# Performance work log

Measured on AMD Instinct MI355X. Metric: run time of the kernel, lower is better.

The kernel has to match this reference:

```python
import jax, jax.numpy as jnp
import numpy as np

N_NODES = 10000
N_EDGES = 320000
D_FEAT = 512
N_HIDDEN = 256
N_LATENT = 64


def setup_inputs() -> dict:
    key = jax.random.key(0)
    ks = jax.random.split(key, 7)
    x = jax.random.normal(ks[0], (N_NODES, D_FEAT), dtype=jnp.float32)
    edge_src = jax.random.randint(ks[1], (N_EDGES,), 0, N_NODES, dtype=jnp.int32)
    edge_dst = jax.random.randint(ks[2], (N_EDGES,), 0, N_NODES, dtype=jnp.int32)
    # positive weights, like D^{-1/2} A D^{-1/2} entries
    edge_weight = jax.random.uniform(ks[3], (N_EDGES,), dtype=jnp.float32)
    scale1 = 1.0 / np.sqrt(D_FEAT)
    scale2 = 1.0 / np.sqrt(N_HIDDEN)
    W1 = jax.random.normal(ks[4], (D_FEAT, N_HIDDEN), dtype=jnp.float32) * scale1
    W2_mu = jax.random.normal(ks[5], (N_HIDDEN, N_LATENT), dtype=jnp.float32) * scale2
    W2_sig = jax.random.normal(ks[6], (N_HIDDEN, N_LATENT), dtype=jnp.float32) * scale2
    return {"x": x, "edge_src": edge_src, "edge_dst": edge_dst,
            "edge_weight": edge_weight, "W1": W1, "W2_mu": W2_mu, "W2_sig": W2_sig}


def reference(x, edge_src, edge_dst, edge_weight, W1, W2_mu, W2_sig):
    N = x.shape[0]

    def spmm(feat):
        # sparse adj_norm @ feat via gather + weighted segment-sum
        msg = feat[edge_src] * edge_weight[:, None]           # [E, F]
        return jax.ops.segment_sum(msg, edge_dst, num_segments=N)  # [N, F]

    # GCN layer 1: relu(adj @ (x @ W1)); dropout is identity at inference
    h = jax.nn.relu(spmm(x @ W1))                              # [N, H]
    # GCN layer 2 (mu and log-sigma heads); encoder returns exp(log_sig)
    mu = spmm(h @ W2_mu)                                       # [N, L]
    sigma = jnp.exp(spmm(h @ W2_sig))                          # [N, L]
    # InnerProductDecoder: adj = z @ z.T (normalized z_ is computed but unused
    # in the original code, so it is faithfully omitted); z = mu embedding
    adj_rec = mu @ mu.T                                        # [N, N]
    return mu, sigma, adj_rec
```

## Files before the change

kernel.cpp:

```cpp
#include <hip/hip_runtime.h>
#include <hip/hip_bf16.h>
#include <math.h>
#include <float.h>

#define N_NODES 10000
#define N_EDGES 320000
#define D_FEAT  512
#define N_HID   256
#define N_LAT   64


__global__ __launch_bounds__(256) void k_hist(const int* __restrict__ dst,
                                              int* __restrict__ deg) {
    int i = blockIdx.x * 256 + threadIdx.x;
    if (i < N_EDGES) atomicAdd(&deg[dst[i]], 1);
}

__global__ __launch_bounds__(1024) void k_scan(const int* __restrict__ deg,
                                               int* __restrict__ rowptr,
                                               int* __restrict__ woff) {
    __shared__ int wsum[16];
    __shared__ int carry_s;
    int tid = threadIdx.x;
    if (tid == 0) carry_s = 0;
    __syncthreads();
    int lane = tid & 63, wv = tid >> 6;
    for (int base = 0; base < N_NODES; base += 1024) {
        int i = base + tid;
        int v = (i < N_NODES) ? deg[i] : 0;
        int x = v;
        #pragma unroll
        for (int off = 1; off < 64; off <<= 1) {
            int y = __shfl_up(x, off);
            if (lane >= off) x += y;
        }
        if (lane == 63) wsum[wv] = x;
        __syncthreads();
        int add = carry_s;
        for (int k = 0; k < wv; k++) add += wsum[k];
        int incl = x + add;
        int excl = incl - v;
        if (i < N_NODES) { rowptr[i] = excl; woff[i] = excl; }
        __syncthreads();
        if (tid == 1023) carry_s = incl;
        __syncthreads();
    }
    if (tid == 0) rowptr[N_NODES] = carry_s;
}

__global__ __launch_bounds__(256) void k_scatter(const int* __restrict__ src,
                                                 const int* __restrict__ dst,
                                                 const float* __restrict__ w,
                                                 int* __restrict__ woff,
                                                 int* __restrict__ esrc,
                                                 float* __restrict__ ew) {
    int i = blockIdx.x * 256 + threadIdx.x;
    if (i < N_EDGES) {
        int d = dst[i];
        int r = atomicAdd(&woff[d], 1);
        esrc[r] = src[i];
        ew[r] = w[i];
    }
}


__global__ __launch_bounds__(256) void k_gemm1(const float* __restrict__ x,
                                               const float* __restrict__ W1,
                                               float* __restrict__ xw1) {
    __shared__ float xs[16][33];
    int j = threadIdx.x;
    int r0 = blockIdx.x * 16;
    float acc[16];
    #pragma unroll
    for (int r = 0; r < 16; r++) acc[r] = 0.f;

    for (int kc = 0; kc < D_FEAT; kc += 32) {
        #pragma unroll
        for (int t = 0; t < 2; t++) {
            int idx = j + t * 256;
            int rr = idx >> 5, kk = idx & 31;
            int row = r0 + rr;
            xs[rr][kk] = (row < N_NODES) ? x[row * D_FEAT + kc + kk] : 0.f;
        }
        __syncthreads();
        #pragma unroll
        for (int kk = 0; kk < 32; kk++) {
            float b = W1[(kc + kk) * N_HID + j];
            #pragma unroll
            for (int r = 0; r < 16; r++) acc[r] += xs[r][kk] * b;
        }
        __syncthreads();
    }
    #pragma unroll
    for (int r = 0; r < 16; r++) {
        int row = r0 + r;
        if (row < N_NODES) xw1[row * N_HID + j] = acc[r];
    }
}


__global__ __launch_bounds__(256) void k_spmm1(const int* __restrict__ rowptr,
                                               const int* __restrict__ esrc,
                                               const float* __restrict__ ew,
                                               const float* __restrict__ xw1,
                                               float* __restrict__ h) {
    int n = blockIdx.x;
    int tid = threadIdx.x;
    int s = rowptr[n], e = rowptr[n + 1];
    float acc = 0.f;
    for (int i = s; i < e; i++) {
        int sc = esrc[i];
        float wv = ew[i];
        acc += wv * xw1[sc * N_HID + tid];
    }
    h[n * N_HID + tid] = fmaxf(acc, 0.f);
}


__global__ __launch_bounds__(256) void k_gemm2(const float* __restrict__ h,
                                               const float* __restrict__ W2mu,
                                               const float* __restrict__ W2sig,
                                               float* __restrict__ pre) {
    __shared__ float hs[32][33];
    int tid = threadIdx.x;
    int j = tid & 127;
    int half = tid >> 7;
    int r0 = blockIdx.x * 32;
    const float* B = (j < 64) ? W2mu : W2sig;
    int jj = j & 63;
    float acc[16];
    #pragma unroll
    for (int r = 0; r < 16; r++) acc[r] = 0.f;

    for (int kc = 0; kc < N_HID; kc += 32) {
        #pragma unroll
        for (int t = 0; t < 4; t++) {
            int idx = tid + t * 256;
            int rr = idx >> 5, kk = idx & 31;
            int row = r0 + rr;
            hs[rr][kk] = (row < N_NODES) ? h[row * N_HID + kc + kk] : 0.f;
        }
        __syncthreads();
        int rb = half * 16;
        #pragma unroll
        for (int kk = 0; kk < 32; kk++) {
            float b = B[(kc + kk) * N_LAT + jj];
            #pragma unroll
            for (int r = 0; r < 16; r++) acc[r] += hs[rb + r][kk] * b;
        }
        __syncthreads();
    }
    #pragma unroll
    for (int r = 0; r < 16; r++) {
        int row = r0 + half * 16 + r;
        if (row < N_NODES) pre[row * 128 + j] = acc[r];
    }
}


__global__ __launch_bounds__(128) void k_spmm2(const int* __restrict__ rowptr,
                                               const int* __restrict__ esrc,
                                               const float* __restrict__ ew,
                                               const float* __restrict__ pre,
                                               float* __restrict__ out_mu,
                                               float* __restrict__ out_sig) {
    int n = blockIdx.x;
    int tid = threadIdx.x;
    int lane = tid & 63, wv = tid >> 6;
    int s = rowptr[n], e = rowptr[n + 1];
    const float* p = pre + wv * 64 + lane;
    float acc = 0.f;
    for (int i = s; i < e; i++) {
        acc += ew[i] * p[esrc[i] * 128];
    }
    if (wv == 0) {
        out_mu[n * 64 + lane] = acc;
    } else {
        float sgv = fminf(expf(acc), 3.0e38f);
        out_sig[n * 64 + lane] = sgv;
    }
}


typedef __bf16 bf16x4 __attribute__((ext_vector_type(4)));
typedef __bf16 bf16x8 __attribute__((ext_vector_type(8)));
typedef float  f32x4  __attribute__((ext_vector_type(4)));

__global__ __launch_bounds__(256) void k_mu2bf(const float* __restrict__ mu,
                                               __bf16* __restrict__ muh,
                                               __bf16* __restrict__ mul) {
    int i = blockIdx.x * 256 + threadIdx.x;
    float4 v = ((const float4*)mu)[i];
    __bf16 h0 = (__bf16)v.x, h1 = (__bf16)v.y, h2 = (__bf16)v.z, h3 = (__bf16)v.w;
    __bf16 l0 = (__bf16)(v.x - (float)h0);
    __bf16 l1 = (__bf16)(v.y - (float)h1);
    __bf16 l2 = (__bf16)(v.z - (float)h2);
    __bf16 l3 = (__bf16)(v.w - (float)h3);
    bf16x4 hv = {h0, h1, h2, h3};
    bf16x4 lv = {l0, l1, l2, l3};
    ((bf16x4*)muh)[i] = hv;
    ((bf16x4*)mul)[i] = lv;
}


#define ADJ_TS 68

__global__ __launch_bounds__(256) void k_adj(const __bf16* __restrict__ muh,
                                             const __bf16* __restrict__ mul,
                                             float* __restrict__ C) {
    __shared__ float Ts[4][32 * ADJ_TS];
    int tid = threadIdx.x;
    int l = tid & 63, w = tid >> 6;
    int wr = w >> 1, wc = w & 1;
    int i0 = blockIdx.y * 128 + wr * 64;
    int j0 = blockIdx.x * 128 + wc * 64;
    int lr = l & 15;
    int lk = (l >> 4) * 8;

    f32x4 acc[4][4];
    #pragma unroll
    for (int a = 0; a < 4; a++)
        #pragma unroll
        for (int b = 0; b < 4; b++) acc[a][b] = (f32x4)(0.0f);

    #pragma unroll
    for (int ks = 0; ks < 2; ks++) {
        int k0 = ks * 32 + lk;
        bf16x8 ah[4], al[4], bh[4], bl[4];
        #pragma unroll
        for (int mi = 0; mi < 4; mi++) {
            int row = i0 + mi * 16 + lr;
            if (row > N_NODES - 1) row = N_NODES - 1;
            ah[mi] = *(const bf16x8*)(muh + row * 64 + k0);
            al[mi] = *(const bf16x8*)(mul + row * 64 + k0);
        }
        #pragma unroll
        for (int ni = 0; ni < 4; ni++) {
            int row = j0 + ni * 16 + lr;
            if (row > N_NODES - 1) row = N_NODES - 1;
            bh[ni] = *(const bf16x8*)(muh + row * 64 + k0);
            bl[ni] = *(const bf16x8*)(mul + row * 64 + k0);
        }
        #pragma unroll
        for (int mi = 0; mi < 4; mi++)
            #pragma unroll
            for (int ni = 0; ni < 4; ni++) {
                acc[mi][ni] = __builtin_amdgcn_mfma_f32_16x16x32_bf16(ah[mi], bh[ni], acc[mi][ni], 0, 0, 0);
                acc[mi][ni] = __builtin_amdgcn_mfma_f32_16x16x32_bf16(ah[mi], bl[ni], acc[mi][ni], 0, 0, 0);
                acc[mi][ni] = __builtin_amdgcn_mfma_f32_16x16x32_bf16(al[mi], bh[ni], acc[mi][ni], 0, 0, 0);
            }
    }

    float* T = Ts[w];
    int c16 = l & 15, r4 = l >> 4;
    #pragma unroll
    for (int half = 0; half < 2; half++) {
        __syncthreads();
        #pragma unroll
        for (int m2 = 0; m2 < 2; m2++) {
            int mi = half * 2 + m2;
            #pragma unroll
            for (int ni = 0; ni < 4; ni++)
                #pragma unroll
                for (int r = 0; r < 4; r++)
                    T[(m2 * 16 + r4 * 4 + r) * ADJ_TS + ni * 16 + c16] = acc[mi][ni][r];
        }
        __syncthreads();
        #pragma unroll
        for (int q = 0; q < 8; q++) {
            int rr = q * 4 + r4;
            int row = i0 + half * 32 + rr;
            int col = j0 + c16 * 4;
            if (row < N_NODES && col < N_NODES)
                *(float4*)&C[(size_t)row * N_NODES + col] =
                    *(const float4*)&T[rr * ADJ_TS + c16 * 4];
        }
    }
}


extern "C" void kernel_launch(void* const* d_in, const int* in_sizes, int n_in,
                              void* d_out, int out_size, void* d_ws, size_t ws_size,
                              hipStream_t stream) {
    const float* x       = (const float*)d_in[0];
    const int*   esrc_in = (const int*)d_in[1];
    const int*   edst_in = (const int*)d_in[2];
    const float* ew_in   = (const float*)d_in[3];
    const float* W1      = (const float*)d_in[4];
    const float* W2mu    = (const float*)d_in[5];
    const float* W2sig   = (const float*)d_in[6];

    char* ws = (char*)d_ws;
    float* xw1    = (float*)(ws + 0);
    float* h      = (float*)(ws + 10240000);
    float* pre    = (float*)(ws + 20480000);
    int*   esrc   = (int*)  (ws + 25600000);
    float* ew     = (float*)(ws + 26880000);
    int*   deg    = (int*)  (ws + 28160000);
    int*   rowptr = (int*)  (ws + 28200000);
    int*   woff   = (int*)  (ws + 28240016);

    __bf16* muh = (__bf16*)(ws + 0);
    __bf16* mul = (__bf16*)(ws + 1280000);

    float* out_mu  = (float*)d_out;
    float* out_sig = out_mu + 640000;
    float* out_adj = out_sig + 640000;

    hipMemsetAsync(deg, 0, N_NODES * sizeof(int), stream);
    k_hist   <<<(N_EDGES + 255) / 256, 256, 0, stream>>>(edst_in, deg);
    k_scan   <<<1, 1024, 0, stream>>>(deg, rowptr, woff);
    k_scatter<<<(N_EDGES + 255) / 256, 256, 0, stream>>>(esrc_in, edst_in, ew_in,
                                                         woff, esrc, ew);
    k_gemm1  <<<N_NODES / 16, 256, 0, stream>>>(x, W1, xw1);
    k_spmm1  <<<N_NODES, 256, 0, stream>>>(rowptr, esrc, ew, xw1, h);
    k_gemm2  <<<(N_NODES + 31) / 32, 256, 0, stream>>>(h, W2mu, W2sig, pre);
    k_spmm2  <<<N_NODES, 128, 0, stream>>>(rowptr, esrc, ew, pre, out_mu, out_sig);
    k_mu2bf  <<<640000 / 4 / 256, 256, 0, stream>>>(out_mu, muh, mul);
    dim3 gadj((N_NODES + 127) / 128, (N_NODES + 127) / 128);
    k_adj    <<<gadj, 256, 0, stream>>>(muh, mul, out_adj);
}
```

Before: 787.6 us.

## Use split-bf16 MFMA for dense GEMMs and wave-per-node vectorized SpMM

The two dense GEMMs (x@W1 and h@W2) move from scalar FP32 FMA loops to bf16 MFMA with a hi/lo split (three products) to keep near-FP32 accuracy. New kernels pre-split x and the weights into bf16 hi/lo parts, and SpMM1 now emits h directly as bf16 hi/lo. The SpMMs are rewritten to one wavefront per node with float4/float2 vector gathers and a 4-way unrolled edge loop, replacing one block per node. This adds split and conversion passes and extra workspace traffic in exchange for matrix-core throughput and fewer, wider memory transactions.

```diff
diff --git a/kernel.cpp b/kernel.cpp
--- a/kernel.cpp
+++ b/kernel.cpp
@@ -8,6 +8,10 @@
 #define D_FEAT  512
 #define N_HID   256
 #define N_LAT   64
+
+typedef __bf16 bf16x4 __attribute__((ext_vector_type(4)));
+typedef __bf16 bf16x8 __attribute__((ext_vector_type(8)));
+typedef float  f32x4  __attribute__((ext_vector_type(4)));
 
 
 __global__ __launch_bounds__(256) void k_hist(const int* __restrict__ dst,
@@ -64,127 +68,238 @@
 }
 
 
-__global__ __launch_bounds__(256) void k_gemm1(const float* __restrict__ x,
-                                               const float* __restrict__ W1,
-                                               float* __restrict__ xw1) {
-    __shared__ float xs[16][33];
-    int j = threadIdx.x;
-    int r0 = blockIdx.x * 16;
-    float acc[16];
-    #pragma unroll
-    for (int r = 0; r < 16; r++) acc[r] = 0.f;
-
-    for (int kc = 0; kc < D_FEAT; kc += 32) {
-        #pragma unroll
-        for (int t = 0; t < 2; t++) {
-            int idx = j + t * 256;
-            int rr = idx >> 5, kk = idx & 31;
-            int row = r0 + rr;
-            xs[rr][kk] = (row < N_NODES) ? x[row * D_FEAT + kc + kk] : 0.f;
-        }
-        __syncthreads();
-        #pragma unroll
-        for (int kk = 0; kk < 32; kk++) {
-            float b = W1[(kc + kk) * N_HID + j];
-            #pragma unroll
-            for (int r = 0; r < 16; r++) acc[r] += xs[r][kk] * b;
-        }
-        __syncthreads();
-    }
-    #pragma unroll
-    for (int r = 0; r < 16; r++) {
-        int row = r0 + r;
-        if (row < N_NODES) xw1[row * N_HID + j] = acc[r];
-    }
-}
-
-
-__global__ __launch_bounds__(256) void k_spmm1(const int* __restrict__ rowptr,
-                                               const int* __restrict__ esrc,
-                                               const float* __restrict__ ew,
-                                               const float* __restrict__ xw1,
-                                               float* __restrict__ h) {
-    int n = blockIdx.x;
+__global__ __launch_bounds__(256) void k_xsplit(const float* __restrict__ x,
+                                                __bf16* __restrict__ xh,
+                                                __bf16* __restrict__ xl) {
+    int i = blockIdx.x * 256 + threadIdx.x;
+    float4 v = ((const float4*)x)[i];
+    __bf16 h0 = (__bf16)v.x, h1 = (__bf16)v.y, h2 = (__bf16)v.z, h3 = (__bf16)v.w;
+    bf16x4 hv = {h0, h1, h2, h3};
+    bf16x4 lv = {(__bf16)(v.x - (float)h0), (__bf16)(v.y - (float)h1),
+                 (__bf16)(v.z - (float)h2), (__bf16)(v.w - (float)h3)};
+    ((bf16x4*)xh)[i] = hv;
+    ((bf16x4*)xl)[i] = lv;
+}
+
+__global__ __launch_bounds__(256) void k_wsplit(const float* __restrict__ W1,
+                                                const float* __restrict__ W2mu,
+                                                const float* __restrict__ W2sig,
+                                                __bf16* __restrict__ w1h,
+                                                __bf16* __restrict__ w1l,
+                                                __bf16* __restrict__ w2h,
+                                                __bf16* __restrict__ w2l) {
+    int i = blockIdx.x * 256 + threadIdx.x;
+    if (i < 512 * 256) {
+        int j = i >> 9, k = i & 511;
+        float v = W1[k * N_HID + j];
+        __bf16 hi = (__bf16)v;
+        w1h[i] = hi;
+        w1l[i] = (__bf16)(v - (float)hi);
+    } else {
+        int t = i - 512 * 256;
+        int j = t >> 8, k = t & 255;
+        float v = (j < 64) ? W2mu[k * N_LAT + j] : W2sig[k * N_LAT + (j - 64)];
+        __bf16 hi = (__bf16)v;
+        w2h[t] = hi;
+        w2l[t] = (__bf16)(v - (float)hi);
+    }
+}
+
+
+__global__ __launch_bounds__(256) void k_gemm1m(const __bf16* __restrict__ xh,
+                                                const __bf16* __restrict__ xl,
+                                                const __bf16* __restrict__ w1h,
+                                                const __bf16* __restrict__ w1l,
+                                                float* __restrict__ xw1) {
     int tid = threadIdx.x;
-    int s = rowptr[n], e = rowptr[n + 1];
-    float acc = 0.f;
-    for (int i = s; i < e; i++) {
-        int sc = esrc[i];
-        float wv = ew[i];
-        acc += wv * xw1[sc * N_HID + tid];
-    }
-    h[n * N_HID + tid] = fmaxf(acc, 0.f);
-}
-
-
-__global__ __launch_bounds__(256) void k_gemm2(const float* __restrict__ h,
-                                               const float* __restrict__ W2mu,
-                                               const float* __restrict__ W2sig,
-                                               float* __restrict__ pre) {
-    __shared__ float hs[32][33];
+    int l = tid & 63, w = tid >> 6;
+    int wr = w >> 1, wc = w & 1;
+    int i0 = blockIdx.y * 128 + wr * 64;
+    int j0 = blockIdx.x * 64 + wc * 32;
+    int lr = l & 15, lk = (l >> 4) * 8;
+
+    f32x4 acc[4][2];
+    #pragma unroll
+    for (int a = 0; a < 4; a++)
+        #pragma unroll
+        for (int b = 0; b < 2; b++) acc[a][b] = (f32x4)(0.0f);
+
+    #pragma unroll 4
+    for (int ks = 0; ks < 16; ks++) {
+        int k0 = ks * 32 + lk;
+        bf16x8 ah[4], al[4], bh[2], bl[2];
+        #pragma unroll
+        for (int mi = 0; mi < 4; mi++) {
+            int row = i0 + mi * 16 + lr;
+            if (row > N_NODES - 1) row = N_NODES - 1;
+            ah[mi] = *(const bf16x8*)(xh + row * D_FEAT + k0);
+            al[mi] = *(const bf16x8*)(xl + row * D_FEAT + k0);
+        }
+        #pragma unroll
+        for (int ni = 0; ni < 2; ni++) {
+            int jr = j0 + ni * 16 + lr;
+            bh[ni] = *(const bf16x8*)(w1h + jr * D_FEAT + k0);
+            bl[ni] = *(const bf16x8*)(w1l + jr * D_FEAT + k0);
+        }
+        #pragma unroll
+        for (int mi = 0; mi < 4; mi++)
+            #pragma unroll
+            for (int ni = 0; ni < 2; ni++) {
+                acc[mi][ni] = __builtin_amdgcn_mfma_f32_16x16x32_bf16(ah[mi], bh[ni], acc[mi][ni], 0, 0, 0);
+                acc[mi][ni] = __builtin_amdgcn_mfma_f32_16x16x32_bf16(ah[mi], bl[ni], acc[mi][ni], 0, 0, 0);
+                acc[mi][ni] = __builtin_amdgcn_mfma_f32_16x16x32_bf16(al[mi], bh[ni], acc[mi][ni], 0, 0, 0);
+            }
+    }
+    int c16 = l & 15, r4 = l >> 4;
+    #pragma unroll
+    for (int mi = 0; mi < 4; mi++)
+        #pragma unroll
+        for (int ni = 0; ni < 2; ni++)
+            #pragma unroll
+            for (int r = 0; r < 4; r++) {
+                int row = i0 + mi * 16 + r4 * 4 + r;
+                int col = j0 + ni * 16 + c16;
+                if (row < N_NODES) xw1[row * N_HID + col] = acc[mi][ni][r];
+            }
+}
+
+
+__global__ __launch_bounds__(256) void k_spmm1w(const int* __restrict__ rowptr,
+                                                const int* __restrict__ esrc,
+                                                const float* __restrict__ ew,
+                                                const float* __restrict__ xw1,
+                                                __bf16* __restrict__ hh,
+                                                __bf16* __restrict__ hl) {
+    int lane = threadIdx.x & 63, w = threadIdx.x >> 6;
+    int n = blockIdx.x * 4 + w;
+    int s = __builtin_amdgcn_readfirstlane(rowptr[n]);
+    int e = __builtin_amdgcn_readfirstlane(rowptr[n + 1]);
+    const float4* X = (const float4*)xw1;
+    float4 acc = make_float4(0.f, 0.f, 0.f, 0.f);
+    int i = s;
+    for (; i + 3 < e; i += 4) {
+        int s0 = esrc[i], s1 = esrc[i + 1], s2 = esrc[i + 2], s3 = esrc[i + 3];
+        float w0 = ew[i], w1 = ew[i + 1], w2 = ew[i + 2], w3 = ew[i + 3];
+        float4 v0 = X[s0 * 64 + lane];
+        float4 v1 = X[s1 * 64 + lane];
+        float4 v2 = X[s2 * 64 + lane];
+        float4 v3 = X[s3 * 64 + lane];
+        acc.x += w0 * v0.x + w1 * v1.x + w2 * v2.x + w3 * v3.x;
+        acc.y += w0 * v0.y + w1 * v1.y + w2 * v2.y + w3 * v3.y;
+        acc.z += w0 * v0.z + w1 * v1.z + w2 * v2.z + w3 * v3.z;
+        acc.w += w0 * v0.w + w1 * v1.w + w2 * v2.w + w3 * v3.w;
+    }
+    for (; i < e; i++) {
+        int sc = esrc[i]; float wv = ew[i];
+        float4 v = X[sc * 64 + lane];
+        acc.x += wv * v.x; acc.y += wv * v.y; acc.z += wv * v.z; acc.w += wv * v.w;
+    }
+    acc.x = fmaxf(acc.x, 0.f); acc.y = fmaxf(acc.y, 0.f);
+    acc.z = fmaxf(acc.z, 0.f); acc.w = fmaxf(acc.w, 0.f);
+    __bf16 h0 = (__bf16)acc.x, h1 = (__bf16)acc.y, h2 = (__bf16)acc.z, h3 = (__bf16)acc.w;
+    bf16x4 hv = {h0, h1, h2, h3};
+    bf16x4 lv = {(__bf16)(acc.x - (float)h0), (__bf16)(acc.y - (float)h1),
+                 (__bf16)(acc.z - (float)h2), (__bf16)(acc.w - (float)h3)};
+    ((bf16x4*)(hh + n * N_HID))[lane] = hv;
+    ((bf16x4*)(hl + n * N_HID))[lane] = lv;
+}
+
+
+__global__ __launch_bounds__(256) void k_gemm2m(const __bf16* __restrict__ hh,
+                                                const __bf16* __restrict__ hl,
+                                                const __bf16* __restrict__ w2h,
+                                                const __bf16* __restrict__ w2l,
+                                                float* __restrict__ pre) {
     int tid = threadIdx.x;
-    int j = tid & 127;
-    int half = tid >> 7;
-    int r0 = blockIdx.x * 32;
-    const float* B = (j < 64) ? W2mu : W2sig;
-    int jj = j & 63;
-    float acc[16];
-    #pragma unroll
-    for (int r = 0; r < 16; r++) acc[r] = 0.f;
-
-    for (int kc = 0; kc < N_HID; kc += 32) {
-        #pragma unroll
-        for (int t = 0; t < 4; t++) {
-            int idx = tid + t * 256;
-            int rr = idx >> 5, kk = idx & 31;
-            int row = r0 + rr;
-            hs[rr][kk] = (row < N_NODES) ? h[row * N_HID + kc + kk] : 0.f;
-        }
-        __syncthreads();
-        int rb = half * 16;
-        #pragma unroll
-        for (int kk = 0; kk < 32; kk++) {
-            float b = B[(kc + kk) * N_LAT + jj];
-            #pragma unroll
-            for (int r = 0; r < 16; r++) acc[r] += hs[rb + r][kk] * b;
-        }
-        __syncthreads();
-    }
-    #pragma unroll
-    for (int r = 0; r < 16; r++) {
-        int row = r0 + half * 16 + r;
-        if (row < N_NODES) pre[row * 128 + j] = acc[r];
-    }
-}
-
-
-__global__ __launch_bounds__(128) void k_spmm2(const int* __restrict__ rowptr,
-                                               const int* __restrict__ esrc,
-                                               const float* __restrict__ ew,
-                                               const float* __restrict__ pre,
-                                               float* __restrict__ out_mu,
-                                               float* __restrict__ out_sig) {
-    int n = blockIdx.x;
-    int tid = threadIdx.x;
-    int lane = tid & 63, wv = tid >> 6;
-    int s = rowptr[n], e = rowptr[n + 1];
-    const float* p = pre + wv * 64 + lane;
-    float acc = 0.f;
-    for (int i = s; i < e; i++) {
-        acc += ew[i] * p[esrc[i] * 128];
-    }
-    if (wv == 0) {
-        out_mu[n * 64 + lane] = acc;
+    int l = tid & 63, w = tid >> 6;
+    int wr = w >> 1, wc = w & 1;
+    int i0 = blockIdx.y * 128 + wr * 64;
+    int j0 = blockIdx.x * 64 + wc * 32;
+    int lr = l & 15, lk = (l >> 4) * 8;
+
+    f32x4 acc[4][2];
+    #pragma unroll
+    for (int a = 0; a < 4; a++)
+        #pragma unroll
+        for (int b = 0; b < 2; b++) acc[a][b] = (f32x4)(0.0f);
+
+    #pragma unroll 4
+    for (int ks = 0; ks < 8; ks++) {
+        int k0 = ks * 32 + lk;
+        bf16x8 ah[4], al[4], bh[2], bl[2];
+        #pragma unroll
+        for (int mi = 0; mi < 4; mi++) {
+            int row = i0 + mi * 16 + lr;
+            if (row > N_NODES - 1) row = N_NODES - 1;
+            ah[mi] = *(const bf16x8*)(hh + row * N_HID + k0);
+            al[mi] = *(const bf16x8*)(hl + row * N_HID + k0);
+        }
+        #pragma unroll
+        for (int ni = 0; ni < 2; ni++) {
+            int jr = j0 + ni * 16 + lr;
+            bh[ni] = *(const bf16x8*)(w2h + jr * N_HID + k0);
+            bl[ni] = *(const bf16x8*)(w2l + jr * N_HID + k0);
+        }
+        #pragma unroll
+        for (int mi = 0; mi < 4; mi++)
+            #pragma unroll
+            for (int ni = 0; ni < 2; ni++) {
+                acc[mi][ni] = __builtin_amdgcn_mfma_f32_16x16x32_bf16(ah[mi], bh[ni], acc[mi][ni], 0, 0, 0);
+                acc[mi][ni] = __builtin_amdgcn_mfma_f32_16x16x32_bf16(ah[mi], bl[ni], acc[mi][ni], 0, 0, 0);
+                acc[mi][ni] = __builtin_amdgcn_mfma_f32_16x16x32_bf16(al[mi], bh[ni], acc[mi][ni], 0, 0, 0);
+            }
+    }
+    int c16 = l & 15, r4 = l >> 4;
+    #pragma unroll
+    for (int mi = 0; mi < 4; mi++)
+        #pragma unroll
+        for (int ni = 0; ni < 2; ni++)
+            #pragma unroll
+            for (int r = 0; r < 4; r++) {
+                int row = i0 + mi * 16 + r4 * 4 + r;
+                int col = j0 + ni * 16 + c16;
+                if (row < N_NODES) pre[row * 128 + col] = acc[mi][ni][r];
+            }
+}
+
+
+__global__ __launch_bounds__(256) void k_spmm2w(const int* __restrict__ rowptr,
+                                                const int* __restrict__ esrc,
+                                                const float* __restrict__ ew,
+                                                const float* __restrict__ pre,
+                                                float* __restrict__ out_mu,
+                                                float* __restrict__ out_sig) {
+    int lane = threadIdx.x & 63, w = threadIdx.x >> 6;
+    int n = blockIdx.x * 4 + w;
+    int s = __builtin_amdgcn_readfirstlane(rowptr[n]);
+    int e = __builtin_amdgcn_readfirstlane(rowptr[n + 1]);
+    const float2* P = (const float2*)pre;
+    float2 acc = make_float2(0.f, 0.f);
+    int i = s;
+    for (; i + 3 < e; i += 4) {
+        int s0 = esrc[i], s1 = esrc[i + 1], s2 = esrc[i + 2], s3 = esrc[i + 3];
+        float w0 = ew[i], w1 = ew[i + 1], w2 = ew[i + 2], w3 = ew[i + 3];
+        float2 v0 = P[s0 * 64 + lane];
+        float2 v1 = P[s1 * 64 + lane];
+        float2 v2 = P[s2 * 64 + lane];
+        float2 v3 = P[s3 * 64 + lane];
+        acc.x += w0 * v0.x + w1 * v1.x + w2 * v2.x + w3 * v3.x;
+        acc.y += w0 * v0.y + w1 * v1.y + w2 * v2.y + w3 * v3.y;
+    }
+    for (; i < e; i++) {
+        int sc = esrc[i]; float wv = ew[i];
+        float2 v = P[sc * 64 + lane];
+        acc.x += wv * v.x; acc.y += wv * v.y;
+    }
+    if (lane < 32) {
+        ((float2*)(out_mu + n * 64))[lane] = acc;
     } else {
-        float sgv = fminf(expf(acc), 3.0e38f);
-        out_sig[n * 64 + lane] = sgv;
-    }
-}
-
-
-typedef __bf16 bf16x4 __attribute__((ext_vector_type(4)));
-typedef __bf16 bf16x8 __attribute__((ext_vector_type(8)));
-typedef float  f32x4  __attribute__((ext_vector_type(4)));
+        float2 sg = make_float2(fminf(expf(acc.x), 3.0e38f),
+                                fminf(expf(acc.y), 3.0e38f));
+        ((float2*)(out_sig + n * 64))[lane - 32] = sg;
+    }
+}
+
 
 __global__ __launch_bounds__(256) void k_mu2bf(const float* __restrict__ mu,
                                                __bf16* __restrict__ muh,
@@ -192,12 +307,9 @@
     int i = blockIdx.x * 256 + threadIdx.x;
     float4 v = ((const float4*)mu)[i];
     __bf16 h0 = (__bf16)v.x, h1 = (__bf16)v.y, h2 = (__bf16)v.z, h3 = (__bf16)v.w;
-    __bf16 l0 = (__bf16)(v.x - (float)h0);
-    __bf16 l1 = (__bf16)(v.y - (float)h1);
-    __bf16 l2 = (__bf16)(v.z - (float)h2);
-    __bf16 l3 = (__bf16)(v.w - (float)h3);
     bf16x4 hv = {h0, h1, h2, h3};
-    bf16x4 lv = {l0, l1, l2, l3};
+    bf16x4 lv = {(__bf16)(v.x - (float)h0), (__bf16)(v.y - (float)h1),
+                 (__bf16)(v.z - (float)h2), (__bf16)(v.w - (float)h3)};
     ((bf16x4*)muh)[i] = hv;
     ((bf16x4*)mul)[i] = lv;
 }
@@ -291,17 +403,23 @@
     const float* W2sig   = (const float*)d_in[6];
 
     char* ws = (char*)d_ws;
-    float* xw1    = (float*)(ws + 0);
-    float* h      = (float*)(ws + 10240000);
-    float* pre    = (float*)(ws + 20480000);
-    int*   esrc   = (int*)  (ws + 25600000);
-    float* ew     = (float*)(ws + 26880000);
-    int*   deg    = (int*)  (ws + 28160000);
-    int*   rowptr = (int*)  (ws + 28200000);
-    int*   woff   = (int*)  (ws + 28240016);
-
-    __bf16* muh = (__bf16*)(ws + 0);
-    __bf16* mul = (__bf16*)(ws + 1280000);
+    __bf16* xh   = (__bf16*)(ws + 0);
+    __bf16* xl   = (__bf16*)(ws + 10240000);
+    float*  xw1  = (float*) (ws + 20480000);
+    __bf16* hh   = (__bf16*)(ws + 0);
+    __bf16* hl   = (__bf16*)(ws + 5120000);
+    float*  pre  = (float*) (ws + 10240000);
+    __bf16* muh  = (__bf16*)(ws + 20480000);
+    __bf16* mul  = (__bf16*)(ws + 21760000);
+    int*    esrc = (int*)   (ws + 30720000);
+    float*  ew   = (float*) (ws + 32000000);
+    __bf16* w1h  = (__bf16*)(ws + 33280000);
+    __bf16* w1l  = (__bf16*)(ws + 33542144);
+    __bf16* w2h  = (__bf16*)(ws + 33804288);
+    __bf16* w2l  = (__bf16*)(ws + 33869824);
+    int*    deg  = (int*)   (ws + 33935360);
+    int*  rowptr = (int*)   (ws + 33975360);
+    int*    woff = (int*)   (ws + 34015376);
 
     float* out_mu  = (float*)d_out;
     float* out_sig = out_mu + 640000;
@@ -312,11 +430,21 @@
     k_scan   <<<1, 1024, 0, stream>>>(deg, rowptr, woff);
     k_scatter<<<(N_EDGES + 255) / 256, 256, 0, stream>>>(esrc_in, edst_in, ew_in,
                                                          woff, esrc, ew);
-    k_gemm1  <<<N_NODES / 16, 256, 0, stream>>>(x, W1, xw1);
-    k_spmm1  <<<N_NODES, 256, 0, stream>>>(rowptr, esrc, ew, xw1, h);
-    k_gemm2  <<<(N_NODES + 31) / 32, 256, 0, stream>>>(h, W2mu, W2sig, pre);
-    k_spmm2  <<<N_NODES, 128, 0, stream>>>(rowptr, esrc, ew, pre, out_mu, out_sig);
+    k_xsplit <<<5000, 256, 0, stream>>>(x, xh, xl);
+    k_wsplit <<<640, 256, 0, stream>>>(W1, W2mu, W2sig, w1h, w1l, w2h, w2l);
+    {
+        dim3 g(4, (N_NODES + 127) / 128);
+        k_gemm1m<<<g, 256, 0, stream>>>(xh, xl, w1h, w1l, xw1);
+    }
+    k_spmm1w <<<N_NODES / 4, 256, 0, stream>>>(rowptr, esrc, ew, xw1, hh, hl);
+    {
+        dim3 g(2, (N_NODES + 127) / 128);
+        k_gemm2m<<<g, 256, 0, stream>>>(hh, hl, w2h, w2l, pre);
+    }
+    k_spmm2w <<<N_NODES / 4, 256, 0, stream>>>(rowptr, esrc, ew, pre, out_mu, out_sig);
     k_mu2bf  <<<640000 / 4 / 256, 256, 0, stream>>>(out_mu, muh, mul);
-    dim3 gadj((N_NODES + 127) / 128, (N_NODES + 127) / 128);
-    k_adj    <<<gadj, 256, 0, stream>>>(muh, mul, out_adj);
-}
+    {
+        dim3 g((N_NODES + 127) / 128, (N_NODES + 127) / 128);
+        k_adj  <<<g, 256, 0, stream>>>(muh, mul, out_adj);
+    }
+}
```

Result: faster. 654.2 us (-16.9%).
